# Optimization experiments

Hardware: AMD Instinct MI355X
Metric: run time of the kernel (lower is better)

Reference implementation:

```python
import jax, jax.numpy as jnp
import numpy as np

D_IN = 1024
D_KQ = 1024
D_V = 1024


def _xavier(key, shape):
    fan_in, fan_out = shape
    limit = float(np.sqrt(6.0 / (fan_in + fan_out)))
    return jax.random.uniform(key, shape, jnp.float32, -limit, limit)


def setup_inputs() -> dict:
    key = jax.random.key(0)
    ks = jax.random.split(key, 8)
    x_1 = jax.random.normal(ks[0], (8, 2048, D_IN), jnp.float32)
    x_2 = jax.random.normal(ks[1], (8, 2048, D_IN), jnp.float32)
    return {
        "x_1": x_1,
        "x_2": x_2,
        "W_query_1": _xavier(ks[2], (D_IN, D_KQ)),
        "W_key_1": _xavier(ks[3], (D_IN, D_KQ)),
        "W_value_1": _xavier(ks[4], (D_IN, D_V)),
        "W_query_2": _xavier(ks[5], (D_IN, D_KQ)),
        "W_key_2": _xavier(ks[6], (D_IN, D_KQ)),
        "W_value_2": _xavier(ks[7], (D_IN, D_V)),
    }


def _cross_attn(x_q, x_kv, W_q, W_k, W_v):
    # x_q: [B, Sq, d_in], x_kv: [B, Sk, d_in]
    q = jnp.einsum("bsd,de->bse", x_q, W_q)   # [B, Sq, d_kq]
    k = jnp.einsum("btd,de->bte", x_kv, W_k)  # [B, Sk, d_kq]
    v = jnp.einsum("btd,de->bte", x_kv, W_v)  # [B, Sk, d_v]
    scores = jnp.einsum("bse,bte->bst", q, k) / jnp.sqrt(jnp.asarray(D_KQ, q.dtype))
    w = jax.nn.softmax(scores, axis=-1)        # [B, Sq, Sk]
    return jnp.einsum("bst,bte->bse", w, v)    # [B, Sq, d_v]


def reference(x_1, x_2, W_query_1, W_key_1, W_value_1, W_query_2, W_key_2, W_value_2):
    # context_vec_2: queries from x_1 (W_query_1), keys/values from x_2 (W_key_2, W_value_2)
    context_vec_2 = _cross_attn(x_1, x_2, W_query_1, W_key_2, W_value_2)
    # context_vec_1: queries from x_2 (W_query_2), keys/values from x_1 (W_key_1, W_value_1)
    context_vec_1 = _cross_attn(x_2, x_1, W_query_2, W_key_1, W_value_1)
    return (context_vec_1, context_vec_2)
```

## Files before the change

kernel.cpp:

```cpp
#include <hip/hip_runtime.h>

typedef _Float16 half8 __attribute__((ext_vector_type(8)));
typedef _Float16 half4 __attribute__((ext_vector_type(4)));
typedef float f4 __attribute__((ext_vector_type(4)));

__device__ __forceinline__ void gload16(const void* g, void* l) {
    __builtin_amdgcn_global_load_lds(
        (const __attribute__((address_space(1))) void*)g,
        (__attribute__((address_space(3))) void*)l, 16, 0, 0);
}
#define BAR()   __builtin_amdgcn_s_barrier()
#define PRIO(x) __builtin_amdgcn_s_setprio(x)
#define LGKM0() do { asm volatile("s_waitcnt lgkmcnt(0)" ::: "memory"); \
                     __builtin_amdgcn_sched_barrier(0); } while (0)

__device__ __forceinline__ int swzb(int row, int c_half) {
    return (row << 7) + ((c_half << 1) ^ ((row & 7) << 4));
}

__global__ void transpose_cast6(const float* __restrict__ W0, const float* __restrict__ W1,
                                const float* __restrict__ W2, const float* __restrict__ W3,
                                const float* __restrict__ W4, const float* __restrict__ W5,
                                _Float16* __restrict__ Wt)
{
    const float* Ws[6] = {W0, W1, W2, W3, W4, W5};
    const float* W = Ws[blockIdx.z];
    _Float16* O = Wt + (size_t)blockIdx.z * (1024u * 1024u);

    __shared__ _Float16 t[64][72];
    const int tid = threadIdx.x;
    const int n0 = blockIdx.x * 64;
    const int k0 = blockIdx.y * 64;

    #pragma unroll
    for (int i = 0; i < 4; ++i) {
        int idx = tid + i * 256;
        int r = idx >> 4;
        int c4 = idx & 15;
        f4 v = *(const f4*)(W + (size_t)(k0 + r) * 1024 + n0 + c4 * 4);
        #pragma unroll
        for (int j = 0; j < 4; ++j) t[r][c4 * 4 + j] = (_Float16)v[j];
    }
    __syncthreads();
    #pragma unroll
    for (int i = 0; i < 4; ++i) {
        int idx = tid + i * 256;
        int r = idx >> 4;
        int c4 = idx & 15;
        half4 h;
        #pragma unroll
        for (int j = 0; j < 4; ++j) h[j] = t[c4 * 4 + j][r];
        *(half4*)(O + (size_t)(n0 + r) * 1024 + k0 + c4 * 4) = h;
    }
}

__global__ void cast2_f32_f16(const float* __restrict__ a, const float* __restrict__ b,
                              _Float16* __restrict__ oa, _Float16* __restrict__ ob)
{
    const float* in  = blockIdx.y ? b : a;
    _Float16*   out = blockIdx.y ? ob : oa;
    const size_t stride = (size_t)gridDim.x * 256 * 8;
    for (size_t i = ((size_t)blockIdx.x * 256 + threadIdx.x) * 8; i < 16777216ull; i += stride) {
        f4 v0 = *(const f4*)(in + i);
        f4 v1 = *(const f4*)(in + i + 4);
        half8 h;
        #pragma unroll
        for (int j = 0; j < 4; ++j) { h[j] = (_Float16)v0[j]; h[4 + j] = (_Float16)v1[j]; }
        *(half8*)(out + i) = h;
    }
}

template<int OMODE>
__global__ __launch_bounds__(512, 2)
void gemm8p(const _Float16* __restrict__ Ain, const _Float16* __restrict__ Btin,
            void* __restrict__ Cout, int lda, int ldb, int ldc, int K,
            long sAz, long sBz, long sCz, float scale)
{
    __shared__ alignas(16) _Float16 lds[2][4][8192];

    const int nwg = gridDim.x * gridDim.y * gridDim.z;
    const int lid = blockIdx.x + gridDim.x * (blockIdx.y + gridDim.y * blockIdx.z);
    const int cpx = nwg >> 3;
    const int sw  = (lid & 7) * cpx + (lid >> 3);
    const int bx  = sw % gridDim.x;
    const int tmp = sw / gridDim.x;
    const int by  = tmp % gridDim.y;
    const int bz  = tmp / gridDim.y;

    const int tid = threadIdx.x, lane = tid & 63, wid = tid >> 6;
    const int wm = wid >> 2, wn = wid & 3;
    const int n0 = bx * 256, m0 = by * 256;

    const _Float16* A  = Ain  + (size_t)bz * sAz;
    const _Float16* Bt = Btin + (size_t)bz * sBz;
    const int KT = K >> 6;

    auto stageHalf = [&](int buf, int reg, const _Float16* src, int ld, int row0, int kt) {
        #pragma unroll
        for (int j = 0; j < 2; ++j) {
            int D = j * 8192 + wid * 1024 + lane * 16;
            int r = D >> 7;
            int c = (D & 127) ^ ((r & 7) << 4);
            gload16(src + (size_t)(row0 + r) * ld + kt * 64 + (c >> 1),
                    &lds[buf][reg][j * 4096 + wid * 512]);
        }
    };

    f4 acc[8][4];
    #pragma unroll
    for (int i = 0; i < 8; ++i)
        #pragma unroll
        for (int j = 0; j < 4; ++j)
            acc[i][j] = f4{0.f, 0.f, 0.f, 0.f};

    half8 a0[4][2], a1[4][2], b[2][2];

    const int lr = lane & 15, lk = (lane >> 4) * 8;
    const int areg  = wm;
    const int breg  = 2 + (wn >> 1);
    const int brow0 = (wn & 1) * 64;

    stageHalf(0, 0, A,  lda, m0,       0);
    stageHalf(0, 1, A,  lda, m0 + 128, 0);
    stageHalf(0, 2, Bt, ldb, n0,       0);
    stageHalf(0, 3, Bt, ldb, n0 + 128, 0);
    if (KT > 1) {
        stageHalf(1, 0, A, lda, m0,       1);
        stageHalf(1, 1, A, lda, m0 + 128, 1);
    }
    asm volatile("s_waitcnt vmcnt(4)" ::: "memory");
    BAR();

    for (int t = 0; t < KT; ++t) {
        const int buf = t & 1;
        const char* LA = (const char*)lds[buf][areg];
        const char* LB = (const char*)lds[buf][breg];

        #pragma unroll
        for (int mf = 0; mf < 4; ++mf)
            #pragma unroll
            for (int kk = 0; kk < 2; ++kk)
                a0[mf][kk] = *(const half8*)(LA + swzb(mf * 16 + lr, kk * 32 + lk));
        #pragma unroll
        for (int nf = 0; nf < 2; ++nf)
            #pragma unroll
            for (int kk = 0; kk < 2; ++kk)
                b[nf][kk] = *(const half8*)(LB + swzb(brow0 + nf * 16 + lr, kk * 32 + lk));
        if (t + 1 < KT) stageHalf(buf ^ 1, 2, Bt, ldb, n0, t + 1);
        asm volatile("s_waitcnt lgkmcnt(8)" ::: "memory");
        BAR(); LGKM0(); PRIO(1);
        #pragma unroll
        for (int mf = 0; mf < 4; ++mf)
            #pragma unroll
            for (int nf = 0; nf < 2; ++nf)
                #pragma unroll
                for (int kk = 0; kk < 2; ++kk)
                    acc[mf][nf] = __builtin_amdgcn_mfma_f32_16x16x32_f16(a0[mf][kk], b[nf][kk], acc[mf][nf], 0, 0, 0);
        PRIO(0); BAR();

        #pragma unroll
        for (int mf = 0; mf < 4; ++mf)
            #pragma unroll
            for (int kk = 0; kk < 2; ++kk)
                a1[mf][kk] = *(const half8*)(LA + swzb(64 + mf * 16 + lr, kk * 32 + lk));
        if (t + 1 < KT) stageHalf(buf ^ 1, 3, Bt, ldb, n0 + 128, t + 1);
        BAR(); LGKM0(); PRIO(1);
        #pragma unroll
        for (int mf = 0; mf < 4; ++mf)
            #pragma unroll
            for (int nf = 0; nf < 2; ++nf)
                #pragma unroll
                for (int kk = 0; kk < 2; ++kk)
                    acc[4 + mf][nf] = __builtin_amdgcn_mfma_f32_16x16x32_f16(a1[mf][kk], b[nf][kk], acc[4 + mf][nf], 0, 0, 0);
        PRIO(0); BAR();

        #pragma unroll
        for (int nf = 0; nf < 2; ++nf)
            #pragma unroll
            for (int kk = 0; kk < 2; ++kk)
                b[nf][kk] = *(const half8*)(LB + swzb(brow0 + 32 + nf * 16 + lr, kk * 32 + lk));
        if (t + 2 < KT) stageHalf(buf, 0, A, lda, m0, t + 2);
        BAR(); LGKM0(); PRIO(1);
        #pragma unroll
        for (int mf = 0; mf < 4; ++mf)
            #pragma unroll
            for (int nf = 0; nf < 2; ++nf)
                #pragma unroll
                for (int kk = 0; kk < 2; ++kk)
                    acc[4 + mf][2 + nf] = __builtin_amdgcn_mfma_f32_16x16x32_f16(a1[mf][kk], b[nf][kk], acc[4 + mf][2 + nf], 0, 0, 0);
        PRIO(0); BAR();

        if (t + 2 < KT) stageHalf(buf, 1, A, lda, m0 + 128, t + 2);
        BAR(); PRIO(1);
        #pragma unroll
        for (int mf = 0; mf < 4; ++mf)
            #pragma unroll
            for (int nf = 0; nf < 2; ++nf)
                #pragma unroll
                for (int kk = 0; kk < 2; ++kk)
                    acc[mf][2 + nf] = __builtin_amdgcn_mfma_f32_16x16x32_f16(a0[mf][kk], b[nf][kk], acc[mf][2 + nf], 0, 0, 0);
        PRIO(0);
        if (t + 2 < KT) { asm volatile("s_waitcnt vmcnt(4)" ::: "memory"); }
        else            { asm volatile("s_waitcnt vmcnt(0)" ::: "memory"); }
        BAR();
    }

    if constexpr (OMODE == 0) {
        _Float16* C = (_Float16*)Cout + (size_t)bz * sCz;
        #pragma unroll
        for (int qm = 0; qm < 2; ++qm)
            #pragma unroll
            for (int mf = 0; mf < 4; ++mf)
                #pragma unroll
                for (int rr = 0; rr < 4; ++rr) {
                    size_t row = (size_t)(m0 + wm * 128 + qm * 64 + mf * 16 + (lane >> 4) * 4 + rr);
                    #pragma unroll
                    for (int qn = 0; qn < 2; ++qn)
                        #pragma unroll
                        for (int nf = 0; nf < 2; ++nf)
                            C[row * ldc + n0 + wn * 64 + qn * 32 + nf * 16 + lr] =
                                (_Float16)(acc[qm * 4 + mf][qn * 2 + nf][rr] * scale);
                }
    } else if constexpr (OMODE == 1) {
        float* C = (float*)Cout + (size_t)bz * sCz;
        #pragma unroll
        for (int qm = 0; qm < 2; ++qm)
            #pragma unroll
            for (int mf = 0; mf < 4; ++mf)
                #pragma unroll
                for (int rr = 0; rr < 4; ++rr) {
                    size_t row = (size_t)(m0 + wm * 128 + qm * 64 + mf * 16 + (lane >> 4) * 4 + rr);
                    #pragma unroll
                    for (int qn = 0; qn < 2; ++qn)
                        #pragma unroll
                        for (int nf = 0; nf < 2; ++nf)
                            C[row * ldc + n0 + wn * 64 + qn * 32 + nf * 16 + lr] =
                                acc[qm * 4 + mf][qn * 2 + nf][rr] * scale;
                }
    } else {
        _Float16* C = (_Float16*)Cout;
        const size_t bofs = (size_t)(m0 >> 11) * (1024ull * 2048ull);
        #pragma unroll
        for (int qn = 0; qn < 2; ++qn)
            #pragma unroll
            for (int nf = 0; nf < 2; ++nf) {
                size_t e = (size_t)(n0 + wn * 64 + qn * 32 + nf * 16 + lr);
                #pragma unroll
                for (int qm = 0; qm < 2; ++qm)
                    #pragma unroll
                    for (int mf = 0; mf < 4; ++mf) {
                        int t0 = (m0 + wm * 128 + qm * 64 + mf * 16 + (lane >> 4) * 4) & 2047;
                        half4 h;
                        #pragma unroll
                        for (int rr = 0; rr < 4; ++rr) h[rr] = (_Float16)acc[qm * 4 + mf][qn * 2 + nf][rr];
                        *(half4*)(C + bofs + e * 2048 + t0) = h;
                    }
            }
    }
}

__global__ void softmax_rows(_Float16* __restrict__ S)
{
    const int wid  = threadIdx.x >> 6;
    const int lane = threadIdx.x & 63;
    const size_t row = (size_t)blockIdx.x * 4 + wid;
    _Float16* p = S + row * 2048;

    float v[32];
    #pragma unroll
    for (int i = 0; i < 4; ++i) {
        half8 h = *(const half8*)(p + i * 512 + lane * 8);
        #pragma unroll
        for (int j = 0; j < 8; ++j) v[i * 8 + j] = (float)h[j];
    }
    float m = -1e30f;
    #pragma unroll
    for (int t = 0; t < 32; ++t) m = fmaxf(m, v[t]);
    #pragma unroll
    for (int mask = 1; mask < 64; mask <<= 1) m = fmaxf(m, __shfl_xor(m, mask));

    float s = 0.f;
    #pragma unroll
    for (int t = 0; t < 32; ++t) { v[t] = __expf(v[t] - m); s += v[t]; }
    #pragma unroll
    for (int mask = 1; mask < 64; mask <<= 1) s += __shfl_xor(s, mask);
    const float r = 1.0f / s;

    #pragma unroll
    for (int i = 0; i < 4; ++i) {
        half8 h;
        #pragma unroll
        for (int j = 0; j < 8; ++j) h[j] = (_Float16)(v[i * 8 + j] * r);
        *(half8*)(p + i * 512 + lane * 8) = h;
    }
}

extern "C" void kernel_launch(void* const* d_in, const int* in_sizes, int n_in,
                              void* d_out, int out_size, void* d_ws, size_t ws_size,
                              hipStream_t stream)
{
    const float* x1 = (const float*)d_in[0];
    const float* x2 = (const float*)d_in[1];

    char* ws = (char*)d_ws;
    _Float16* Wt  = (_Float16*)ws;
    _Float16* X1h = (_Float16*)(ws + 12582912L);
    _Float16* X2h = (_Float16*)(ws + 12582912L + 33554432L);
    _Float16* Q   = (_Float16*)(ws + 12582912L + 2 * 33554432L);
    _Float16* Kk  = (_Float16*)(ws + 12582912L + 3 * 33554432L);
    _Float16* Vt  = (_Float16*)(ws + 12582912L + 4 * 33554432L);
    _Float16* S   = (_Float16*)(ws + 12582912L + 5 * 33554432L);

    transpose_cast6<<<dim3(16, 16, 6), 256, 0, stream>>>(
        (const float*)d_in[2], (const float*)d_in[3], (const float*)d_in[4],
        (const float*)d_in[5], (const float*)d_in[6], (const float*)d_in[7], Wt);

    cast2_f32_f16<<<dim3(2048, 2), 256, 0, stream>>>(x1, x2, X1h, X2h);

    for (int d = 0; d < 2; ++d) {
        const _Float16* xq  = (d == 0) ? X1h : X2h;
        const _Float16* xkv = (d == 0) ? X2h : X1h;
        const _Float16* wtq = Wt + (size_t)((d == 0) ? 0 : 3) * 1048576;
        const _Float16* wtk = Wt + (size_t)((d == 0) ? 4 : 1) * 1048576;
        const _Float16* wtv = Wt + (size_t)((d == 0) ? 5 : 2) * 1048576;
        float* outp = (float*)d_out + ((d == 0) ? 16777216L : 0L);

        gemm8p<0><<<dim3(4, 64, 1), 512, 0, stream>>>(xq,  wtq, Q,  1024, 1024, 1024, 1024, 0, 0, 0, 1.f);
        gemm8p<0><<<dim3(4, 64, 1), 512, 0, stream>>>(xkv, wtk, Kk, 1024, 1024, 1024, 1024, 0, 0, 0, 1.f);
        gemm8p<2><<<dim3(4, 64, 1), 512, 0, stream>>>(xkv, wtv, Vt, 1024, 1024, 0,    1024, 0, 0, 0, 1.f);

        gemm8p<0><<<dim3(8, 8, 8), 512, 0, stream>>>(Q, Kk, S, 1024, 1024, 2048, 1024,
                                                     2048L * 1024, 2048L * 1024, 2048L * 2048, 0.03125f);
        softmax_rows<<<4096, 256, 0, stream>>>(S);

        gemm8p<1><<<dim3(4, 8, 8), 512, 0, stream>>>(S, Vt, outp, 2048, 2048, 1024, 2048,
                                                     2048L * 2048, 2048L * 1024, 2048L * 1024, 1.f);
    }
}
```

Measured before the change: 794.1 us.

## Software-pipeline LDS fragment reads across MFMA phases and drop intra-iteration barriers

```diff
diff --git a/kernel.cpp b/kernel.cpp
--- a/kernel.cpp
+++ b/kernel.cpp
@@ -11,8 +11,10 @@
 }
 #define BAR()   __builtin_amdgcn_s_barrier()
 #define PRIO(x) __builtin_amdgcn_s_setprio(x)
-#define LGKM0() do { asm volatile("s_waitcnt lgkmcnt(0)" ::: "memory"); \
-                     __builtin_amdgcn_sched_barrier(0); } while (0)
+#define LGKMW(n) do { asm volatile("s_waitcnt lgkmcnt(" #n ")" ::: "memory"); \
+                      __builtin_amdgcn_sched_barrier(0); } while (0)
+#define VMW(n)   do { asm volatile("s_waitcnt vmcnt(" #n ")" ::: "memory"); \
+                      __builtin_amdgcn_sched_barrier(0); } while (0)
 
 __device__ __forceinline__ int swzb(int row, int c_half) {
     return (row << 7) + ((c_half << 1) ^ ((row & 7) << 4));
@@ -120,6 +122,57 @@
     const int breg  = 2 + (wn >> 1);
     const int brow0 = (wn & 1) * 64;
 
+    auto readA0 = [&](int b_) {
+        const char* L = (const char*)lds[b_][areg];
+        #pragma unroll
+        for (int mf = 0; mf < 4; ++mf)
+            #pragma unroll
+            for (int kk = 0; kk < 2; ++kk)
+                a0[mf][kk] = *(const half8*)(L + swzb(mf * 16 + lr, kk * 32 + lk));
+    };
+    auto readA1 = [&](int b_) {
+        const char* L = (const char*)lds[b_][areg];
+        #pragma unroll
+        for (int mf = 0; mf < 4; ++mf)
+            #pragma unroll
+            for (int kk = 0; kk < 2; ++kk)
+                a1[mf][kk] = *(const half8*)(L + swzb(64 + mf * 16 + lr, kk * 32 + lk));
+    };
+    auto readB01 = [&](int b_) {
+        const char* L = (const char*)lds[b_][breg];
+        #pragma unroll
+        for (int nf = 0; nf < 2; ++nf)
+            #pragma unroll
+            for (int kk = 0; kk < 2; ++kk)
+                b[nf][kk] = *(const half8*)(L + swzb(brow0 + nf * 16 + lr, kk * 32 + lk));
+    };
+    auto readB23 = [&](int b_) {
+        const char* L = (const char*)lds[b_][breg];
+        #pragma unroll
+        for (int nf = 0; nf < 2; ++nf)
+            #pragma unroll
+            for (int kk = 0; kk < 2; ++kk)
+                b[nf][kk] = *(const half8*)(L + swzb(brow0 + 32 + nf * 16 + lr, kk * 32 + lk));
+    };
+    auto mfmaA0 = [&](int bj) {
+        #pragma unroll
+        for (int mf = 0; mf < 4; ++mf)
+            #pragma unroll
+            for (int nf = 0; nf < 2; ++nf)
+                #pragma unroll
+                for (int kk = 0; kk < 2; ++kk)
+                    acc[mf][bj + nf] = __builtin_amdgcn_mfma_f32_16x16x32_f16(a0[mf][kk], b[nf][kk], acc[mf][bj + nf], 0, 0, 0);
+    };
+    auto mfmaA1 = [&](int bj) {
+        #pragma unroll
+        for (int mf = 0; mf < 4; ++mf)
+            #pragma unroll
+            for (int nf = 0; nf < 2; ++nf)
+                #pragma unroll
+                for (int kk = 0; kk < 2; ++kk)
+                    acc[4 + mf][bj + nf] = __builtin_amdgcn_mfma_f32_16x16x32_f16(a1[mf][kk], b[nf][kk], acc[4 + mf][bj + nf], 0, 0, 0);
+    };
+
     stageHalf(0, 0, A,  lda, m0,       0);
     stageHalf(0, 1, A,  lda, m0 + 128, 0);
     stageHalf(0, 2, Bt, ldb, n0,       0);
@@ -128,81 +181,39 @@
         stageHalf(1, 0, A, lda, m0,       1);
         stageHalf(1, 1, A, lda, m0 + 128, 1);
     }
-    asm volatile("s_waitcnt vmcnt(4)" ::: "memory");
+    VMW(4);
     BAR();
+    readA0(0);
+    readB01(0);
 
     for (int t = 0; t < KT; ++t) {
         const int buf = t & 1;
-        const char* LA = (const char*)lds[buf][areg];
-        const char* LB = (const char*)lds[buf][breg];
-
-        #pragma unroll
-        for (int mf = 0; mf < 4; ++mf)
-            #pragma unroll
-            for (int kk = 0; kk < 2; ++kk)
-                a0[mf][kk] = *(const half8*)(LA + swzb(mf * 16 + lr, kk * 32 + lk));
-        #pragma unroll
-        for (int nf = 0; nf < 2; ++nf)
-            #pragma unroll
-            for (int kk = 0; kk < 2; ++kk)
-                b[nf][kk] = *(const half8*)(LB + swzb(brow0 + nf * 16 + lr, kk * 32 + lk));
+
         if (t + 1 < KT) stageHalf(buf ^ 1, 2, Bt, ldb, n0, t + 1);
-        asm volatile("s_waitcnt lgkmcnt(8)" ::: "memory");
-        BAR(); LGKM0(); PRIO(1);
-        #pragma unroll
-        for (int mf = 0; mf < 4; ++mf)
-            #pragma unroll
-            for (int nf = 0; nf < 2; ++nf)
-                #pragma unroll
-                for (int kk = 0; kk < 2; ++kk)
-                    acc[mf][nf] = __builtin_amdgcn_mfma_f32_16x16x32_f16(a0[mf][kk], b[nf][kk], acc[mf][nf], 0, 0, 0);
-        PRIO(0); BAR();
-
-        #pragma unroll
-        for (int mf = 0; mf < 4; ++mf)
-            #pragma unroll
-            for (int kk = 0; kk < 2; ++kk)
-                a1[mf][kk] = *(const half8*)(LA + swzb(64 + mf * 16 + lr, kk * 32 + lk));
+        LGKMW(0); PRIO(1);
+        mfmaA0(0);
+        PRIO(0);
+        readA1(buf);
+
         if (t + 1 < KT) stageHalf(buf ^ 1, 3, Bt, ldb, n0 + 128, t + 1);
-        BAR(); LGKM0(); PRIO(1);
-        #pragma unroll
-        for (int mf = 0; mf < 4; ++mf)
-            #pragma unroll
-            for (int nf = 0; nf < 2; ++nf)
-                #pragma unroll
-                for (int kk = 0; kk < 2; ++kk)
-                    acc[4 + mf][nf] = __builtin_amdgcn_mfma_f32_16x16x32_f16(a1[mf][kk], b[nf][kk], acc[4 + mf][nf], 0, 0, 0);
-        PRIO(0); BAR();
-
-        #pragma unroll
-        for (int nf = 0; nf < 2; ++nf)
-            #pragma unroll
-            for (int kk = 0; kk < 2; ++kk)
-                b[nf][kk] = *(const half8*)(LB + swzb(brow0 + 32 + nf * 16 + lr, kk * 32 + lk));
+        LGKMW(0); PRIO(1);
+        mfmaA1(0);
+        PRIO(0);
+        readB23(buf);
+        BAR();
+
         if (t + 2 < KT) stageHalf(buf, 0, A, lda, m0, t + 2);
-        BAR(); LGKM0(); PRIO(1);
-        #pragma unroll
-        for (int mf = 0; mf < 4; ++mf)
-            #pragma unroll
-            for (int nf = 0; nf < 2; ++nf)
-                #pragma unroll
-                for (int kk = 0; kk < 2; ++kk)
-                    acc[4 + mf][2 + nf] = __builtin_amdgcn_mfma_f32_16x16x32_f16(a1[mf][kk], b[nf][kk], acc[4 + mf][2 + nf], 0, 0, 0);
-        PRIO(0); BAR();
+        LGKMW(0); PRIO(1);
+        mfmaA1(2);
+        PRIO(0);
 
         if (t + 2 < KT) stageHalf(buf, 1, A, lda, m0 + 128, t + 2);
-        BAR(); PRIO(1);
-        #pragma unroll
-        for (int mf = 0; mf < 4; ++mf)
-            #pragma unroll
-            for (int nf = 0; nf < 2; ++nf)
-                #pragma unroll
-                for (int kk = 0; kk < 2; ++kk)
-                    acc[mf][2 + nf] = __builtin_amdgcn_mfma_f32_16x16x32_f16(a0[mf][kk], b[nf][kk], acc[mf][2 + nf], 0, 0, 0);
+        PRIO(1);
+        mfmaA0(2);
         PRIO(0);
-        if (t + 2 < KT) { asm volatile("s_waitcnt vmcnt(4)" ::: "memory"); }
-        else            { asm volatile("s_waitcnt vmcnt(0)" ::: "memory"); }
+        if (t + 2 < KT) { VMW(4); } else { VMW(0); }
         BAR();
+        if (t + 1 < KT) { readA0(buf ^ 1); readB01(buf ^ 1); }
     }
 
     if constexpr (OMODE == 0) {
```

New measurement: 782.8 us. Within noise of the previous version (-1.4%).
